# Performance work log

Hardware: AMD Instinct MI355X
Metric: run time of the kernel (lower is better)

## Reference

```python
import jax, jax.numpy as jnp
import numpy as np

N, C, T, V = 8, 256, 256, 25
NH = 8
DK = 256           # dk_factor(1.0) * out_channels
DV = 256           # only_temporal_attention -> dv = out_channels
DKH = DK // NH     # 32
DVH = DV // NH     # 32
BN_EPS = 1e-5


def setup_inputs() -> dict:
    key = jax.random.key(0)
    ks = jax.random.split(key, 10)
    return {
        "x": jax.random.normal(ks[0], (N, C, T, V), jnp.float32),
        # pointwise (1,1) qkv conv: weight (2*dk+dv, C), torch conv_init scale
        "qkv_w": jax.random.normal(ks[1], (2 * DK + DV, C), jnp.float32) * (2.0 / (2 * DK + DV)) ** 0.5,
        "qkv_b": jax.random.normal(ks[2], (2 * DK + DV,), jnp.float32) * 0.02,
        # relative key embeddings: (2*frames-1, dk // Nh)
        "key_rel": jax.random.normal(ks[3], (2 * T - 1, DKH), jnp.float32),
        # attn_out pointwise conv: (dv, dv)
        "attn_w": jax.random.normal(ks[4], (DV, DV), jnp.float32) * (1.0 / DV) ** 0.5,
        "attn_b": jax.random.normal(ks[5], (DV,), jnp.float32) * 0.02,
        # BatchNorm2d (eval mode) params / running stats
        "bn_gamma": 1.0 + 0.1 * jax.random.normal(ks[6], (DV,), jnp.float32),
        "bn_beta": 0.1 * jax.random.normal(ks[7], (DV,), jnp.float32),
        "bn_mean": 0.1 * jax.random.normal(ks[8], (DV,), jnp.float32),
        "bn_var": jax.random.uniform(ks[9], (DV,), jnp.float32, minval=0.5, maxval=1.5),
    }


def rel_to_abs(x):
    # x: (B, Nh, L, 2L-1) -> (B, Nh, L, L) via standard pad/reshape/slice trick
    B, Nh, L, _ = x.shape
    x = jnp.pad(x, ((0, 0), (0, 0), (0, 0), (0, 1)))          # (B,Nh,L,2L)
    flat = x.reshape(B, Nh, L * 2 * L)
    flat = jnp.pad(flat, ((0, 0), (0, 0), (0, L - 1)))
    final = flat.reshape(B, Nh, L + 1, 2 * L - 1)
    return final[:, :, :L, L - 1:]


def reference(x, qkv_w, qkv_b, key_rel, attn_w, attn_b, bn_gamma, bn_beta, bn_mean, bn_var):
    n, c, t, v = x.shape
    x_sum = x
    B = n * v
    # (N,C,T,V) -> (N*V, C, T): each joint is an independent temporal sequence
    xr = jnp.transpose(x, (0, 3, 1, 2)).reshape(B, c, t)
    # pointwise qkv conv (kernel (1,1), stride 1)
    qkv = jnp.einsum('bct,oc->bot', xr, qkv_w) + qkv_b[None, :, None]
    q, k, vv = qkv[:, :DK], qkv[:, DK:2 * DK], qkv[:, 2 * DK:]
    q = q.reshape(B, NH, DKH, t) * (DKH ** -0.5)   # scaling applied before rel logits too
    k = k.reshape(B, NH, DKH, t)
    vv = vv.reshape(B, NH, DVH, t)
    # content logits: (B,NH,t,t)
    logits = jnp.einsum('bhdt,bhds->bhts', q, k)
    # relative logits: (B,NH,t,2t-1) -> abs (B,NH,t,t)
    rel = jnp.einsum('bhdt,md->bhtm', q, key_rel)
    logits = logits + rel_to_abs(rel)
    weights = jax.nn.softmax(logits, axis=-1)
    attn = jnp.einsum('bhts,bhds->bhtd', weights, vv)          # (B,NH,t,DVH)
    # combine heads (head-major channel order) -> (B, DV, t)
    attn = jnp.transpose(attn, (0, 1, 3, 2)).reshape(B, DV, t)
    # attn_out pointwise conv
    attn = jnp.einsum('bct,oc->bot', attn, attn_w) + attn_b[None, :, None]
    # (N*V, DV, T) -> (N, DV, T, V)
    attn = attn.reshape(n, v, DV, t).transpose(0, 2, 3, 1)
    # skip connection (in==out, stride==1 -> identity down path)
    result = attn + x_sum
    # BatchNorm2d in eval mode
    inv = bn_gamma / jnp.sqrt(bn_var + BN_EPS)
    result = result * inv[None, :, None, None] + (bn_beta - bn_mean * inv)[None, :, None, None]
    return jax.nn.relu(result)
```

## Files before the change

kernel.cpp:

```cpp
#include <hip/hip_runtime.h>

#define NB 8
#define CC 256
#define TT 256
#define VV 25

typedef unsigned int u32;
typedef unsigned short u16;
typedef __attribute__((ext_vector_type(8))) short s16x8;
typedef __attribute__((ext_vector_type(4))) float f32x4;

__device__ __forceinline__ float bf2f(u16 u) { return __uint_as_float((u32)u << 16); }
__device__ __forceinline__ u16 f2bf(float f) {
    u32 u = __float_as_uint(f);
    u += 0x7fffu + ((u >> 16) & 1u);
    return (u16)(u >> 16);
}
__device__ __forceinline__ u16 f2bf_rtz(float f) { return (u16)(__float_as_uint(f) >> 16); }

__device__ __forceinline__ void gload_lds16(const void* g, void* l) {
    __builtin_amdgcn_global_load_lds(
        (const __attribute__((address_space(1))) u32*)g,
        (__attribute__((address_space(3))) u32*)l, 16, 0, 0);
}

__global__ __launch_bounds__(256) void k_transpose_x(const float* __restrict__ x,
                                                     u16* __restrict__ xT) {
    __shared__ u16 L[25 * 32 * 34];
    const int tid = threadIdx.x;
    const int c0 = blockIdx.x * 32;
    const int t0 = blockIdx.y * 32;
    const int n  = blockIdx.z;
    for (int i = tid; i < 25600; i += 256) {
        int ci = i / 800;
        int rem = i - ci * 800;
        int t = rem / 25;
        int v = rem - t * 25;
        float f = x[(((size_t)(n * CC + c0 + ci)) * TT + t0) * VV + rem];
        L[(v * 32 + t) * 34 + ci] = f2bf(f);
    }
    __syncthreads();
    for (int i = tid; i < 12800; i += 256) {
        int row = i >> 4, cp = i & 15;
        int v = row >> 5, t = row & 31;
        u32 val = *(const u32*)&L[row * 34 + cp * 2];
        *(u32*)&xT[(((size_t)(n * VV + v)) * TT + t0 + t) * CC + c0 + cp * 2] = val;
    }
}

__global__ __launch_bounds__(256) void k_pack_all(const float* __restrict__ qkv_w,
                                                  const float* __restrict__ attn_w,
                                                  const float* __restrict__ qkv_b,
                                                  const float* __restrict__ key_rel,
                                                  u16* __restrict__ Wqk,
                                                  u16* __restrict__ Wv,
                                                  u16* __restrict__ Wo,
                                                  float* __restrict__ bqk,
                                                  u16* __restrict__ krb) {
    const float s = 0.17677669529663687f;
    int g = blockIdx.x * 256 + threadIdx.x;
    if (g < 131072) {
        Wqk[g] = f2bf(qkv_w[g] * (g < 65536 ? s : 1.f));
    } else if (g < 196608) {
        Wv[g - 131072] = f2bf(qkv_w[g]);
    } else if (g < 262144) {
        Wo[g - 196608] = f2bf(attn_w[g - 196608]);
    } else if (g < 262656) {
        int i = g - 262144;
        bqk[i] = qkv_b[i] * (i < 256 ? s : 1.f);
    } else if (g < 279040) {
        int i = g - 262656;
        krb[i] = (i < 511 * 32) ? f2bf(key_rel[i]) : (u16)0;
    }
}

__device__ __forceinline__ void gemm_mainloop(const u16* __restrict__ Arow,
                                              const u16* __restrict__ Brow,
                                              u16* At, u16* Bt,
                                              int wave, int lane, f32x4 acc[4][4]) {
    const int srow = lane >> 2, scol = (lane & 3) * 8;
    const int quad = lane >> 4, l15 = lane & 15;
    for (int k0 = 0; k0 < 256; k0 += 32) {
#pragma unroll
        for (int it = 0; it < 2; ++it) {
            int ch = it * 4 + wave;
            gload_lds16(Arow + (size_t)(ch * 16 + srow) * 256 + k0 + scol, At + ch * 512 + lane * 8);
            gload_lds16(Brow + (size_t)(ch * 16 + srow) * 256 + k0 + scol, Bt + ch * 512 + lane * 8);
        }
        __syncthreads();
        s16x8 af[4], bfr[4];
#pragma unroll
        for (int i = 0; i < 4; ++i)
            af[i] = *(const s16x8*)&At[((wave & 1) * 64 + i * 16 + l15) * 32 + quad * 8];
#pragma unroll
        for (int j = 0; j < 4; ++j)
            bfr[j] = *(const s16x8*)&Bt[((wave >> 1) * 64 + j * 16 + l15) * 32 + quad * 8];
#pragma unroll
        for (int i = 0; i < 4; ++i)
#pragma unroll
            for (int j = 0; j < 4; ++j)
                acc[i][j] = __builtin_amdgcn_mfma_f32_16x16x32_bf16(af[i], bfr[j], acc[i][j], 0, 0, 0);
        __syncthreads();
    }
}

__global__ __launch_bounds__(256) void k_gemm_qk(const u16* __restrict__ xT,
                                                 const u16* __restrict__ Wqk,
                                                 const float* __restrict__ bqk,
                                                 u16* __restrict__ qk_all) {
    __shared__ __align__(16) u16 At[128 * 32];
    __shared__ __align__(16) u16 Bt[128 * 32];
    const int tid = threadIdx.x, wave = tid >> 6, lane = tid & 63;
    const int quad = lane >> 4, l15 = lane & 15;
    const int n0 = blockIdx.x * 128;
    const int m0 = blockIdx.y * 128;
    const int b  = blockIdx.z;
    const u16* Arow = xT + (size_t)b * 65536 + (size_t)m0 * 256;
    const u16* Brow = Wqk + (size_t)n0 * 256;
    f32x4 acc[4][4];
#pragma unroll
    for (int i = 0; i < 4; ++i)
#pragma unroll
        for (int j = 0; j < 4; ++j) acc[i][j] = (f32x4){0.f, 0.f, 0.f, 0.f};
    gemm_mainloop(Arow, Brow, At, Bt, wave, lane, acc);

    u16* ob = qk_all + (size_t)b * 131072;
    const int nb = n0 + (wave >> 1) * 64 + l15;
    float bj[4];
#pragma unroll
    for (int j = 0; j < 4; ++j) bj[j] = bqk[nb + j * 16];
#pragma unroll
    for (int i = 0; i < 4; ++i) {
        int t_i = m0 + (wave & 1) * 64 + i * 16 + quad * 4;
#pragma unroll
        for (int r = 0; r < 4; ++r) {
            u16* orow = ob + (size_t)(t_i + r) * 512 + nb;
#pragma unroll
            for (int j = 0; j < 4; ++j)
                orow[j * 16] = f2bf(acc[i][j][r] + bj[j]);
        }
    }
}

__global__ __launch_bounds__(256) void k_gemm_av(const u16* __restrict__ Wb,
                                                 const float* __restrict__ bias,
                                                 const u16* __restrict__ Bsrc,
                                                 u16* __restrict__ Out) {
    __shared__ __align__(16) u16 At[128 * 32];
    __shared__ __align__(16) u16 Bt[128 * 32];
    const int tid = threadIdx.x, wave = tid >> 6, lane = tid & 63;
    const int quad = lane >> 4, l15 = lane & 15;
    const int n0 = blockIdx.x * 128;
    const int m0 = blockIdx.y * 128;
    const int b  = blockIdx.z;
    const u16* Arow = Wb + (size_t)m0 * 256;
    const u16* Brow = Bsrc + (size_t)b * 65536 + (size_t)n0 * 256;
    f32x4 acc[4][4];
#pragma unroll
    for (int i = 0; i < 4; ++i)
#pragma unroll
        for (int j = 0; j < 4; ++j) acc[i][j] = (f32x4){0.f, 0.f, 0.f, 0.f};
    gemm_mainloop(Arow, Brow, At, Bt, wave, lane, acc);

    u16* ob = Out + (size_t)b * 65536;
    const int nb = n0 + (wave >> 1) * 64 + l15;
#pragma unroll
    for (int i = 0; i < 4; ++i) {
        int o_i = m0 + (wave & 1) * 64 + i * 16 + quad * 4;
#pragma unroll
        for (int r = 0; r < 4; ++r) {
            float bv = bias[o_i + r];
            u16* orow = ob + (size_t)(o_i + r) * 256 + nb;
#pragma unroll
            for (int j = 0; j < 4; ++j)
                orow[j * 16] = f2bf(acc[i][j][r] + bv);
        }
    }
}

__global__ __launch_bounds__(256, 4) void k_attention_mfma(const u16* __restrict__ qk,
                                                           const u16* __restrict__ vb,
                                                           const u16* __restrict__ krb,
                                                           u16* __restrict__ attn) {
    __shared__ __align__(16) u16 RP[4][16 * 280];

    const int tid = threadIdx.x;
    const int bh = blockIdx.x;
    const int b = bh >> 3, h = bh & 7;
    const int wave = tid >> 6, lane = tid & 63;
    const int quad = lane >> 4, l15 = lane & 15;
    const int t0w = blockIdx.y * 64 + wave * 16;
    const int tl = quad * 4;

    u16* rp = &RP[wave][0];
    const u16* qrow = qk + (size_t)b * 131072;
    const u16* vg   = vb + (size_t)bh * 8192;
    const u16* krg  = krb + (size_t)(240 - t0w) * 32;

    s16x8 afrag = *(const s16x8*)(qrow + (size_t)(t0w + l15) * 512 + h * 32 + quad * 8);

#pragma unroll
    for (int j = 0; j < 17; ++j) {
        s16x8 bfrag = *(const s16x8*)(krg + (size_t)(j * 16 + l15) * 32 + quad * 8);
        f32x4 c = {0.f, 0.f, 0.f, 0.f};
        c = __builtin_amdgcn_mfma_f32_16x16x32_bf16(afrag, bfrag, c, 0, 0, 0);
        int col = j * 16 + l15;
        rp[(tl + 0) * 280 + col] = f2bf_rtz(c[0]);
        rp[(tl + 1) * 280 + col] = f2bf_rtz(c[1]);
        rp[(tl + 2) * 280 + col] = f2bf_rtz(c[2]);
        rp[(tl + 3) * 280 + col] = f2bf_rtz(c[3]);
    }

    f32x4 acc[16];
#pragma unroll
    for (int n = 0; n < 16; ++n) {
#pragma unroll
        for (int r = 0; r < 4; ++r) {
            int tlr = tl + r;
            acc[n][r] = bf2f(rp[tlr * 280 + (n * 16 + l15 - tlr + 15)]);
        }
    }
#pragma unroll
    for (int n = 0; n < 16; ++n) {
        s16x8 kf = *(const s16x8*)(qrow + (size_t)(n * 16 + l15) * 512 + 256 + h * 32 + quad * 8);
        acc[n] = __builtin_amdgcn_mfma_f32_16x16x32_bf16(afrag, kf, acc[n], 0, 0, 0);
    }

    float invr[4];
#pragma unroll
    for (int r = 0; r < 4; ++r) {
        float tmp[16];
#pragma unroll
        for (int n = 0; n < 16; ++n) tmp[n] = acc[n][r];
#pragma unroll
        for (int st = 8; st; st >>= 1)
#pragma unroll
            for (int n = 0; n < 8; ++n)
                if (n < st) tmp[n] = fmaxf(tmp[n], tmp[n + st]);
        float m = tmp[0];
#pragma unroll
        for (int off = 1; off < 16; off <<= 1) m = fmaxf(m, __shfl_xor(m, off, 64));
        float sm[16];
#pragma unroll
        for (int n = 0; n < 16; ++n) {
            float e = __expf(acc[n][r] - m);
            acc[n][r] = e;
            sm[n] = e;
        }
#pragma unroll
        for (int st = 8; st; st >>= 1)
#pragma unroll
            for (int n = 0; n < 8; ++n)
                if (n < st) sm[n] += sm[n + st];
        float s = sm[0];
#pragma unroll
        for (int off = 1; off < 16; off <<= 1) s += __shfl_xor(s, off, 64);
        invr[r] = 1.f / s;
    }
#pragma unroll
    for (int n = 0; n < 16; ++n) {
#pragma unroll
        for (int r = 0; r < 4; ++r)
            rp[(tl + r) * 280 + n * 16 + l15] = f2bf_rtz(acc[n][r] * invr[r]);
    }

#pragma unroll
    for (int j = 0; j < 2; ++j) {
        f32x4 o = {0.f, 0.f, 0.f, 0.f};
#pragma unroll
        for (int ks = 0; ks < 8; ++ks) {
            s16x8 a  = *(const s16x8*)&rp[l15 * 280 + ks * 32 + quad * 8];
            s16x8 bv = *(const s16x8*)(vg + (size_t)(j * 16 + l15) * 256 + ks * 32 + quad * 8);
            o = __builtin_amdgcn_mfma_f32_16x16x32_bf16(a, bv, o, 0, 0, 0);
        }
        u16* ob = attn + ((size_t)b * 256 + t0w + tl) * 256 + h * 32 + j * 16 + l15;
        ob[0]   = f2bf(o[0]);
        ob[256] = f2bf(o[1]);
        ob[512] = f2bf(o[2]);
        ob[768] = f2bf(o[3]);
    }
}

__global__ __launch_bounds__(256) void k_final(const u16* __restrict__ y,
                                               const float* __restrict__ x,
                                               const float* __restrict__ gamma,
                                               const float* __restrict__ beta,
                                               const float* __restrict__ mean,
                                               const float* __restrict__ var,
                                               float* __restrict__ out) {
    __shared__ float tile[1600];
    const int tid = threadIdx.x;
    const int t0 = blockIdx.x * 64;
    const int o  = blockIdx.y;
    const int n  = blockIdx.z;
    float inv = gamma[o] * rsqrtf(var[o] + 1e-5f);
    float sh  = beta[o] - mean[o] * inv;
    for (int p = tid; p < 1600; p += 256) {
        int v = p >> 6, j = p & 63;
        tile[j * VV + v] = bf2f(y[(((size_t)(n * VV + v)) * CC + o) * TT + t0 + j]);
    }
    __syncthreads();
    size_t gbase = (((size_t)(n * CC + o)) * TT + t0) * VV;
    for (int i = tid; i < 1600; i += 256) {
        float val = tile[i] + x[gbase + i];
        val = val * inv + sh;
        out[gbase + i] = fmaxf(val, 0.f);
    }
}

extern "C" void kernel_launch(void* const* d_in, const int* in_sizes, int n_in,
                              void* d_out, int out_size, void* d_ws, size_t ws_size,
                              hipStream_t stream) {
    const float* x        = (const float*)d_in[0];
    const float* qkv_w    = (const float*)d_in[1];
    const float* qkv_b    = (const float*)d_in[2];
    const float* key_rel  = (const float*)d_in[3];
    const float* attn_w   = (const float*)d_in[4];
    const float* attn_b   = (const float*)d_in[5];
    const float* bn_gamma = (const float*)d_in[6];
    const float* bn_beta  = (const float*)d_in[7];
    const float* bn_mean  = (const float*)d_in[8];
    const float* bn_var   = (const float*)d_in[9];
    float* out = (float*)d_out;

    char* ws = (char*)d_ws;
    u16* xT     = (u16*)ws;
    u16* qk_all = (u16*)(ws + 26214400);
    u16* vb     = (u16*)(ws + 78643200);
    u16* attnT  = (u16*)(ws + 104857600);
    u16* y      = qk_all;

    char* outc = (char*)d_out;
    u16* Wqk   = (u16*)outc;
    u16* Wv    = (u16*)(outc + 262144);
    u16* Wo    = (u16*)(outc + 393216);
    float* bqk = (float*)(outc + 524288);
    u16* krb   = (u16*)(outc + 526336);

    k_pack_all<<<1090, 256, 0, stream>>>(qkv_w, attn_w, qkv_b, key_rel, Wqk, Wv, Wo, bqk, krb);
    k_transpose_x<<<dim3(8, 8, 8), 256, 0, stream>>>(x, xT);
    k_gemm_qk<<<dim3(4, 2, 200), 256, 0, stream>>>(xT, Wqk, bqk, qk_all);
    k_gemm_av<<<dim3(2, 2, 200), 256, 0, stream>>>(Wv, qkv_b + 512, xT, vb);
    k_attention_mfma<<<dim3(1600, 4), 256, 0, stream>>>(qk_all, vb, krb, attnT);
    k_gemm_av<<<dim3(2, 2, 200), 256, 0, stream>>>(Wo, attn_b, attnT, y);
    k_final<<<dim3(4, 256, 8), 256, 0, stream>>>(y, x, bn_gamma, bn_beta, bn_mean, bn_var, out);
}
```

Baseline: 361.2 us.

## Batch global fragment loads, split MFMA accumulators, remap blocks to spread heads

In the attention kernel, the relative-key, key and value fragments are now loaded into register arrays before the MFMA loops, so global load latency overlaps instead of serializing with each MFMA. The PV reduction uses two independent accumulators to break the MFMA dependency chain. The block index is remapped so adjacent blocks cover different batch-joint sequences for the same head. The occupancy hint drops from 4 to 3 blocks per CU to make room for the extra registers, which may lower latency hiding elsewhere.

```diff
diff --git a/kernel.cpp b/kernel.cpp
--- a/kernel.cpp
+++ b/kernel.cpp
@@ -178,15 +178,17 @@
     }
 }
 
-__global__ __launch_bounds__(256, 4) void k_attention_mfma(const u16* __restrict__ qk,
+__global__ __launch_bounds__(256, 3) void k_attention_mfma(const u16* __restrict__ qk,
                                                            const u16* __restrict__ vb,
                                                            const u16* __restrict__ krb,
                                                            u16* __restrict__ attn) {
     __shared__ __align__(16) u16 RP[4][16 * 280];
 
     const int tid = threadIdx.x;
-    const int bh = blockIdx.x;
-    const int b = bh >> 3, h = bh & 7;
+    const int L = blockIdx.x;
+    const int b = (L & 7) * 25 + ((L >> 3) % 25);
+    const int h = L / 200;
+    const int bh = b * 8 + h;
     const int wave = tid >> 6, lane = tid & 63;
     const int quad = lane >> 4, l15 = lane & 15;
     const int t0w = blockIdx.y * 64 + wave * 16;
@@ -199,11 +201,14 @@
 
     s16x8 afrag = *(const s16x8*)(qrow + (size_t)(t0w + l15) * 512 + h * 32 + quad * 8);
 
+    s16x8 krf[17];
+#pragma unroll
+    for (int j = 0; j < 17; ++j)
+        krf[j] = *(const s16x8*)(krg + (size_t)(j * 16 + l15) * 32 + quad * 8);
 #pragma unroll
     for (int j = 0; j < 17; ++j) {
-        s16x8 bfrag = *(const s16x8*)(krg + (size_t)(j * 16 + l15) * 32 + quad * 8);
         f32x4 c = {0.f, 0.f, 0.f, 0.f};
-        c = __builtin_amdgcn_mfma_f32_16x16x32_bf16(afrag, bfrag, c, 0, 0, 0);
+        c = __builtin_amdgcn_mfma_f32_16x16x32_bf16(afrag, krf[j], c, 0, 0, 0);
         int col = j * 16 + l15;
         rp[(tl + 0) * 280 + col] = f2bf_rtz(c[0]);
         rp[(tl + 1) * 280 + col] = f2bf_rtz(c[1]);
@@ -211,6 +216,10 @@
         rp[(tl + 3) * 280 + col] = f2bf_rtz(c[3]);
     }
 
+    s16x8 kf[16];
+#pragma unroll
+    for (int n = 0; n < 16; ++n)
+        kf[n] = *(const s16x8*)(qrow + (size_t)(n * 16 + l15) * 512 + 256 + h * 32 + quad * 8);
     f32x4 acc[16];
 #pragma unroll
     for (int n = 0; n < 16; ++n) {
@@ -221,10 +230,8 @@
         }
     }
 #pragma unroll
-    for (int n = 0; n < 16; ++n) {
-        s16x8 kf = *(const s16x8*)(qrow + (size_t)(n * 16 + l15) * 512 + 256 + h * 32 + quad * 8);
-        acc[n] = __builtin_amdgcn_mfma_f32_16x16x32_bf16(afrag, kf, acc[n], 0, 0, 0);
-    }
+    for (int n = 0; n < 16; ++n)
+        acc[n] = __builtin_amdgcn_mfma_f32_16x16x32_bf16(afrag, kf[n], acc[n], 0, 0, 0);
 
     float invr[4];
 #pragma unroll
@@ -266,18 +273,24 @@
 
 #pragma unroll
     for (int j = 0; j < 2; ++j) {
-        f32x4 o = {0.f, 0.f, 0.f, 0.f};
-#pragma unroll
-        for (int ks = 0; ks < 8; ++ks) {
-            s16x8 a  = *(const s16x8*)&rp[l15 * 280 + ks * 32 + quad * 8];
-            s16x8 bv = *(const s16x8*)(vg + (size_t)(j * 16 + l15) * 256 + ks * 32 + quad * 8);
-            o = __builtin_amdgcn_mfma_f32_16x16x32_bf16(a, bv, o, 0, 0, 0);
+        s16x8 vf[8], pa[8];
+#pragma unroll
+        for (int ks = 0; ks < 8; ++ks)
+            vf[ks] = *(const s16x8*)(vg + (size_t)(j * 16 + l15) * 256 + ks * 32 + quad * 8);
+#pragma unroll
+        for (int ks = 0; ks < 8; ++ks)
+            pa[ks] = *(const s16x8*)&rp[l15 * 280 + ks * 32 + quad * 8];
+        f32x4 o0 = {0.f, 0.f, 0.f, 0.f}, o1 = {0.f, 0.f, 0.f, 0.f};
+#pragma unroll
+        for (int ks = 0; ks < 8; ks += 2) {
+            o0 = __builtin_amdgcn_mfma_f32_16x16x32_bf16(pa[ks],     vf[ks],     o0, 0, 0, 0);
+            o1 = __builtin_amdgcn_mfma_f32_16x16x32_bf16(pa[ks + 1], vf[ks + 1], o1, 0, 0, 0);
         }
         u16* ob = attn + ((size_t)b * 256 + t0w + tl) * 256 + h * 32 + j * 16 + l15;
-        ob[0]   = f2bf(o[0]);
-        ob[256] = f2bf(o[1]);
-        ob[512] = f2bf(o[2]);
-        ob[768] = f2bf(o[3]);
+        ob[0]   = f2bf(o0[0] + o1[0]);
+        ob[256] = f2bf(o0[1] + o1[1]);
+        ob[512] = f2bf(o0[2] + o1[2]);
+        ob[768] = f2bf(o0[3] + o1[3]);
     }
 }
 
```

Result: no change. 360.3 us (-0.3%).
